# Kernel tuning notes

Hardware: AMD Instinct MI355X
Metric: run time of the kernel (lower is better)

## Reference

```python
import jax, jax.numpy as jnp
import numpy as np
import math

MODEL_DIM = 1024
HEAD_DIM = 64
NUM_HEADS = 16
FF_MULT = 4
FF_DIM = FF_MULT * MODEL_DIM
ATTN_DIM = NUM_HEADS * HEAD_DIM
FUSED_DIMS = (ATTN_DIM, ATTN_DIM, ATTN_DIM, FF_DIM, FF_DIM)


def setup_inputs() -> dict:
    key = jax.random.key(0)
    k_x, k_in, k_attn, k_ff = jax.random.split(key, 4)
    B, S = 2, 2048
    inputs = jax.random.normal(k_x, (B, S, MODEL_DIM), dtype=jnp.float32)
    # LayerNorm affine params (torch defaults: weight=1, bias=0)
    ln_w = jnp.ones((MODEL_DIM,), dtype=jnp.float32)
    ln_b = jnp.zeros((MODEL_DIM,), dtype=jnp.float32)
    # Linear weights stored as [in, out] (equivalent to torch W.T)
    s_in = 1.0 / math.sqrt(MODEL_DIM)
    w_in = jax.random.uniform(k_in, (MODEL_DIM, sum(FUSED_DIMS)), jnp.float32, -s_in, s_in)
    s_a = 1.0 / math.sqrt(ATTN_DIM)
    w_attn = jax.random.uniform(k_attn, (ATTN_DIM, MODEL_DIM), jnp.float32, -s_a, s_a)
    s_f = 1.0 / math.sqrt(FF_DIM)
    w_ff = jax.random.uniform(k_ff, (FF_DIM, MODEL_DIM), jnp.float32, -s_f, s_f)
    return {"inputs": inputs, "ln_w": ln_w, "ln_b": ln_b,
            "w_in": w_in, "w_attn": w_attn, "w_ff": w_ff}


def _layer_norm(x, w, b, eps=1e-5):
    mu = jnp.mean(x, axis=-1, keepdims=True)
    var = jnp.var(x, axis=-1, keepdims=True)
    return (x - mu) * jax.lax.rsqrt(var + eps) * w + b


def reference(inputs, ln_w, ln_b, w_in, w_attn, w_ff):
    B, S, D = inputs.shape
    units = _layer_norm(inputs, ln_w, ln_b)
    proj = units @ w_in                                   # [B,S,3*A+2*F]
    splits = np.cumsum(FUSED_DIMS)[:-1]
    q, k, v, ff, ff_gate = jnp.split(proj, splits, axis=-1)
    # split heads: [B,S,H*d] -> [B,H,S,d]
    def heads(t):
        return t.reshape(B, S, NUM_HEADS, HEAD_DIM).transpose(0, 2, 1, 3)
    q, k, v = heads(q), heads(k), heads(v)
    scale = 1.0 / math.sqrt(HEAD_DIM)
    score = jnp.einsum('bhsd,bhTd->bhsT', q, k) * scale   # [B,H,S,S]
    weight = jax.nn.softmax(score, axis=-1)
    attn = jnp.einsum('bhsT,bhTd->bhsd', weight, v)       # [B,H,S,d]
    concat = attn.transpose(0, 2, 1, 3).reshape(B, S, ATTN_DIM)
    attn_out = concat @ w_attn                            # [B,S,D]
    ff_out = (ff * jax.nn.gelu(ff_gate, approximate=True)) @ w_ff
    return inputs + attn_out + ff_out
```

## Files before the change

kernel.cpp:

```cpp
#include <hip/hip_runtime.h>
#include <hip/hip_bf16.h>
#include <cstdint>
#include <cstddef>

typedef __bf16 bf16;
typedef __bf16 bf16x8 __attribute__((ext_vector_type(8)));
typedef float f32x4 __attribute__((ext_vector_type(4)));

#define MFMA16(a, b, c) __builtin_amdgcn_mfma_f32_16x16x32_bf16(a, b, c, 0, 0, 0)

#define GLOBAL_LOAD_LDS16(gptr, lptr)                                          \
  __builtin_amdgcn_global_load_lds(                                            \
      (const __attribute__((address_space(1))) void*)(gptr),                   \
      (__attribute__((address_space(3))) void*)(lptr), 16, 0, 0)

__global__ void transpose_all(const float* __restrict__ w_in,
                              const float* __restrict__ w_attn,
                              const float* __restrict__ w_ff,
                              bf16* __restrict__ wt_in,
                              bf16* __restrict__ wtcat) {
  __shared__ float t[32][33];
  int id = blockIdx.x;
  const float* src; bf16* dst;
  int srcN, srccol0, LDO, mode, obase, goff, kcol0, ntn;
  if (id < 3072) {
    src = w_in; dst = wt_in; srcN = 11264; srccol0 = 0; LDO = 1024;
    mode = 0; obase = 0; goff = 0; kcol0 = 0; ntn = 96;
  } else if (id < 7168) {
    id -= 3072; src = w_in; dst = wt_in; srcN = 11264; srccol0 = 3072;
    LDO = 1024; mode = 1; obase = 3072; goff = 0; kcol0 = 0; ntn = 128;
  } else if (id < 11264) {
    id -= 7168; src = w_in; dst = wt_in; srcN = 11264; srccol0 = 7168;
    LDO = 1024; mode = 1; obase = 3072; goff = 64; kcol0 = 0; ntn = 128;
  } else if (id < 12288) {
    id -= 11264; src = w_attn; dst = wtcat; srcN = 1024; srccol0 = 0;
    LDO = 5120; mode = 0; obase = 0; goff = 0; kcol0 = 0; ntn = 32;
  } else {
    id -= 12288; src = w_ff; dst = wtcat; srcN = 1024; srccol0 = 0;
    LDO = 5120; mode = 0; obase = 0; goff = 0; kcol0 = 1024; ntn = 32;
  }
  const int n0 = (id % ntn) * 32, k0 = (id / ntn) * 32;
  const int tx = threadIdx.x, ty = threadIdx.y;
  for (int i = ty; i < 32; i += 8)
    t[i][tx] = src[(size_t)(k0 + i) * srcN + srccol0 + n0 + tx];
  __syncthreads();
  for (int i = ty; i < 32; i += 8) {
    int n = n0 + i;
    int orow = mode ? (obase + ((n >> 6) << 7) + goff + (n & 63)) : (obase + n);
    dst[(size_t)orow * LDO + kcol0 + k0 + tx] = (bf16)t[tx][i];
  }
}

__global__ __launch_bounds__(256) void lnorm(const float* __restrict__ x,
                                             const float* __restrict__ w,
                                             const float* __restrict__ b,
                                             bf16* __restrict__ y) {
  const int row = blockIdx.x;
  const int tid = threadIdx.x;
  const float* xr = x + (size_t)row * 1024;
  float4 v = *(const float4*)&xr[tid * 4];
  float s = v.x + v.y + v.z + v.w;
  float ss = v.x * v.x + v.y * v.y + v.z * v.z + v.w * v.w;
  __shared__ float rs[256], rss[256];
  rs[tid] = s; rss[tid] = ss;
  __syncthreads();
  for (int off = 128; off > 0; off >>= 1) {
    if (tid < off) { rs[tid] += rs[tid + off]; rss[tid] += rss[tid + off]; }
    __syncthreads();
  }
  const float mean = rs[0] * (1.f / 1024.f);
  const float var = rss[0] * (1.f / 1024.f) - mean * mean;
  const float rstd = rsqrtf(var + 1e-5f);
  const float* vp = (const float*)&v;
  for (int i = 0; i < 4; i++) {
    int c = tid * 4 + i;
    y[(size_t)row * 1024 + c] = (bf16)((vp[i] - mean) * rstd * w[c] + b[c]);
  }
}

__global__ __launch_bounds__(256) void vtrans(const bf16* __restrict__ proj,
                                              bf16* __restrict__ vt) {
  __shared__ bf16 t[64][80];
  const int tid = threadIdx.x;
  const int s0 = blockIdx.x * 64;
  const int h = blockIdx.y, b = blockIdx.z;
  constexpr size_t LDP = 3072;
  const bf16* src = proj + (size_t)b * 2048 * LDP + 2048 + h * 64;
  {
    int s = tid >> 2, d0 = (tid & 3) * 16;
    *(bf16x8*)&t[s][d0]     = *(const bf16x8*)&src[(size_t)(s0 + s) * LDP + d0];
    *(bf16x8*)&t[s][d0 + 8] = *(const bf16x8*)&src[(size_t)(s0 + s) * LDP + d0 + 8];
  }
  __syncthreads();
  {
    int d = tid >> 2, sb = (tid & 3) * 16;
    bf16* dst = vt + ((size_t)(b * 16 + h) * 64 + d) * 2048 + s0 + sb;
    bf16x8 o0, o1;
    for (int i = 0; i < 8; i++) { o0[i] = t[sb + i][d]; o1[i] = t[sb + 8 + i][d]; }
    *(bf16x8*)&dst[0] = o0;
    *(bf16x8*)&dst[8] = o1;
  }
}

__global__ __launch_bounds__(256) void flash_attn(const bf16* __restrict__ proj,
                                                  const bf16* __restrict__ vt,
                                                  bf16* __restrict__ hcat) {
  __shared__ __align__(16) char smem[50176];
  bf16* Ks = (bf16*)smem;
  bf16* Vs = (bf16*)(smem + 16384);
  bf16* Ps = (bf16*)(smem + 32768);
  const int tid = threadIdx.x;
  const int wave = tid >> 6, lane = tid & 63;
  const int quad = lane >> 4, l16 = lane & 15;
  const int q0 = blockIdx.x * 64;
  const int h = blockIdx.y, b = blockIdx.z;
  constexpr size_t LDP = 3072;
  const bf16* Qb = proj + (size_t)b * 2048 * LDP + h * 64;
  const bf16* Kb = proj + (size_t)b * 2048 * LDP + 1024 + h * 64;
  const bf16* Vt = vt + (size_t)(b * 16 + h) * 64 * 2048;

  const int qrow = q0 + wave * 16 + l16;
  bf16x8 aq0r = *(const bf16x8*)&Qb[(size_t)qrow * LDP + quad * 8];
  bf16x8 aq1r = *(const bf16x8*)&Qb[(size_t)qrow * LDP + 32 + quad * 8];
  bf16x8 aq0, aq1;
#pragma unroll
  for (int i = 0; i < 8; i++) {
    aq0[i] = (bf16)((float)aq0r[i] * 0.125f);
    aq1[i] = (bf16)((float)aq1r[i] * 0.125f);
  }

  f32x4 O[4] = {};
  float lrow[4] = {0.f, 0.f, 0.f, 0.f};

  const int krow = wave * 8 + (lane >> 3);
  const int kq   = ((lane & 7) ^ ((lane >> 3) & 7)) * 8;
  const int kslot = (lane & 7) * 8;
  const int vrow = wave * 4 + (lane >> 4);
  const int vq   = ((lane & 15) ^ ((wave * 4 + (lane >> 4)) & 7)) * 8;
  const int vslot = (lane & 15) * 8;
  const int ks0 = (quad ^ (l16 & 7)) * 8;
  const int ks1 = ((quad + 4) ^ (l16 & 7)) * 8;

  for (int j0 = 0; j0 < 2048; j0 += 128) {
#pragma unroll
    for (int p = 0; p < 4; p++) {
      int kr = p * 32 + krow;
      GLOBAL_LOAD_LDS16(&Kb[(size_t)(j0 + kr) * LDP + kq], &Ks[kr * 64 + kslot]);
      int vr = p * 16 + vrow;
      GLOBAL_LOAD_LDS16(&Vt[(size_t)vr * 2048 + j0 + vq], &Vs[vr * 128 + vslot]);
    }
    __syncthreads();

    f32x4 sa[8];
#pragma unroll
    for (int nt = 0; nt < 8; nt++) {
      bf16x8 bk0 = *(const bf16x8*)&Ks[(nt * 16 + l16) * 64 + ks0];
      bf16x8 bk1 = *(const bf16x8*)&Ks[(nt * 16 + l16) * 64 + ks1];
      f32x4 t = {};
      t = MFMA16(aq0, bk0, t);
      sa[nt] = MFMA16(aq1, bk1, t);
    }

    bf16* Pw = Ps + wave * (16 * 136);
#pragma unroll
    for (int r = 0; r < 4; r++) {
      bf16* pr = &Pw[(quad * 4 + r) * 136];
      float ts = 0.f;
#pragma unroll
      for (int nt = 0; nt < 8; nt++) {
        float p = __expf(sa[nt][r]);
        pr[nt * 16 + l16] = (bf16)p;
        ts += p;
      }
#pragma unroll
      for (int d = 1; d < 16; d <<= 1) ts += __shfl_xor(ts, d, 64);
      lrow[r] += ts;
    }

#pragma unroll
    for (int kg = 0; kg < 4; kg++) {
      bf16x8 aP = *(const bf16x8*)&Pw[l16 * 136 + kg * 32 + quad * 8];
#pragma unroll
      for (int nb = 0; nb < 4; nb++) {
        int vrr = nb * 16 + l16;
        int vsl = (((kg * 4 + quad) ^ (l16 & 7))) * 8;
        bf16x8 bv = *(const bf16x8*)&Vs[vrr * 128 + vsl];
        O[nb] = MFMA16(aP, bv, O[nb]);
      }
    }
    __syncthreads();
  }

#pragma unroll
  for (int r = 0; r < 4; r++) {
    float inv = 1.f / lrow[r];
    size_t row = (size_t)b * 2048 + q0 + wave * 16 + quad * 4 + r;
#pragma unroll
    for (int nb = 0; nb < 4; nb++)
      hcat[row * 5120 + h * 64 + nb * 16 + l16] = (bf16)(O[nb][r] * inv);
  }
}

__global__ __launch_bounds__(256) void gemm_proj(const bf16* __restrict__ A,
                                                 const bf16* __restrict__ Bt,
                                                 bf16* __restrict__ proj,
                                                 bf16* __restrict__ hcat) {
  constexpr int K = 1024, LDC = 136;
  __shared__ __align__(16) char smem[17408];
  bf16* As = (bf16*)smem;
  bf16* Bs = As + 128 * 32;
  bf16* Cs = (bf16*)smem;
  const int tid = threadIdx.x;
  const int wave = tid >> 6, lane = tid & 63;
  const int quad = lane >> 4, l16 = lane & 15;
  constexpr int NM = 4, NN = 4;
  const int wm0 = (wave >> 1) * 64, wn0 = (wave & 1) * 64;
  const size_t rowA0 = (size_t)blockIdx.y * 128;
  const size_t rowB0 = (size_t)blockIdx.x * 128;

  const int srow = wave * 16 + (lane >> 2);
  const int sq = ((lane & 3) ^ ((lane >> 3) & 3)) * 8;
  const int sslot = (lane & 3) * 8;
  const int rslot = (quad ^ ((l16 >> 1) & 3)) * 8;

  f32x4 acc[NM][NN] = {};

  for (int k0 = 0; k0 < K; k0 += 32) {
#pragma unroll
    for (int p = 0; p < 2; p++) {
      int r = p * 64 + srow;
      GLOBAL_LOAD_LDS16(&A[(rowA0 + r) * K + k0 + sq], &As[r * 32 + sslot]);
      GLOBAL_LOAD_LDS16(&Bt[(rowB0 + r) * K + k0 + sq], &Bs[r * 32 + sslot]);
    }
    __syncthreads();
    bf16x8 af[NM], bfr[NN];
#pragma unroll
    for (int i = 0; i < NM; i++)
      af[i] = *(const bf16x8*)&As[(wm0 + i * 16 + l16) * 32 + rslot];
#pragma unroll
    for (int j = 0; j < NN; j++)
      bfr[j] = *(const bf16x8*)&Bs[(wn0 + j * 16 + l16) * 32 + rslot];
#pragma unroll
    for (int i = 0; i < NM; i++)
#pragma unroll
      for (int j = 0; j < NN; j++)
        acc[i][j] = MFMA16(af[i], bfr[j], acc[i][j]);
    __syncthreads();
  }

#pragma unroll
  for (int half = 0; half < 2; half++) {
    if ((wave >> 1) == half) {
#pragma unroll
      for (int i = 0; i < NM; i++)
#pragma unroll
        for (int j = 0; j < NN; j++)
#pragma unroll
          for (int r = 0; r < 4; r++)
            Cs[(i * 16 + quad * 4 + r) * LDC + wn0 + j * 16 + l16] =
                (bf16)acc[i][j][r];
    }
    __syncthreads();
    if (blockIdx.x < 24) {
      const int c0 = (tid & 15) * 8;
#pragma unroll
      for (int it = 0; it < 4; it++) {
        int row = (tid >> 4) + it * 16;
        *(bf16x8*)&proj[(rowA0 + half * 64 + row) * 3072 + rowB0 + c0] =
            *(const bf16x8*)&Cs[row * LDC + c0];
      }
    } else {
      const int T = blockIdx.x - 24;
      const int c0 = (tid & 7) * 8;
#pragma unroll
      for (int p = 0; p < 2; p++) {
        int row = (tid >> 3) + p * 32;
        bf16x8 f = *(const bf16x8*)&Cs[row * LDC + c0];
        bf16x8 g = *(const bf16x8*)&Cs[row * LDC + 64 + c0];
        bf16x8 o;
#pragma unroll
        for (int i = 0; i < 8; i++) {
          float xg = (float)g[i];
          float u = 0.7978845608f * (xg + 0.044715f * xg * xg * xg);
          float gl = xg / (1.f + __expf(-2.f * u));
          o[i] = (bf16)((float)f[i] * gl);
        }
        *(bf16x8*)&hcat[(rowA0 + half * 64 + row) * 5120 + 1024 + T * 64 + c0] = o;
      }
    }
    __syncthreads();
  }
}

__global__ __launch_bounds__(256) void gemm_out(const bf16* __restrict__ A,
                                                const bf16* __restrict__ Bt,
                                                bf16* __restrict__ part) {
  constexpr int LDAB = 5120, LDC = 136;
  __shared__ __align__(16) char smem[17408];
  bf16* As = (bf16*)smem;
  bf16* Bs = As + 128 * 32;
  bf16* Cs = (bf16*)smem;
  const int tid = threadIdx.x;
  const int wave = tid >> 6, lane = tid & 63;
  const int quad = lane >> 4, l16 = lane & 15;
  constexpr int NM = 4, NN = 4;
  const int wm0 = (wave >> 1) * 64, wn0 = (wave & 1) * 64;
  const size_t rowA0 = (size_t)blockIdx.y * 128;
  const size_t rowB0 = (size_t)blockIdx.x * 128;
  const int kbeg = blockIdx.z * 1280, kend = kbeg + 1280;

  const int srow = wave * 16 + (lane >> 2);
  const int sq = ((lane & 3) ^ ((lane >> 3) & 3)) * 8;
  const int sslot = (lane & 3) * 8;
  const int rslot = (quad ^ ((l16 >> 1) & 3)) * 8;

  f32x4 acc[NM][NN] = {};

  for (int k0 = kbeg; k0 < kend; k0 += 32) {
#pragma unroll
    for (int p = 0; p < 2; p++) {
      int r = p * 64 + srow;
      GLOBAL_LOAD_LDS16(&A[(rowA0 + r) * LDAB + k0 + sq], &As[r * 32 + sslot]);
      GLOBAL_LOAD_LDS16(&Bt[(rowB0 + r) * LDAB + k0 + sq], &Bs[r * 32 + sslot]);
    }
    __syncthreads();
    bf16x8 af[NM], bfr[NN];
#pragma unroll
    for (int i = 0; i < NM; i++)
      af[i] = *(const bf16x8*)&As[(wm0 + i * 16 + l16) * 32 + rslot];
#pragma unroll
    for (int j = 0; j < NN; j++)
      bfr[j] = *(const bf16x8*)&Bs[(wn0 + j * 16 + l16) * 32 + rslot];
#pragma unroll
    for (int i = 0; i < NM; i++)
#pragma unroll
      for (int j = 0; j < NN; j++)
        acc[i][j] = MFMA16(af[i], bfr[j], acc[i][j]);
    __syncthreads();
  }

  bf16* dst = part + (size_t)blockIdx.z * (4096 * 1024);
#pragma unroll
  for (int half = 0; half < 2; half++) {
    if ((wave >> 1) == half) {
#pragma unroll
      for (int i = 0; i < NM; i++)
#pragma unroll
        for (int j = 0; j < NN; j++)
#pragma unroll
          for (int r = 0; r < 4; r++)
            Cs[(i * 16 + quad * 4 + r) * LDC + wn0 + j * 16 + l16] =
                (bf16)acc[i][j][r];
    }
    __syncthreads();
    const int c0 = (tid & 15) * 8;
#pragma unroll
    for (int it = 0; it < 4; it++) {
      int row = (tid >> 4) + it * 16;
      *(bf16x8*)&dst[(rowA0 + half * 64 + row) * 1024 + rowB0 + c0] =
          *(const bf16x8*)&Cs[row * LDC + c0];
    }
    __syncthreads();
  }
}

__global__ __launch_bounds__(256) void reduce_out(const float* __restrict__ x,
                                                  const bf16* __restrict__ part,
                                                  float* __restrict__ out) {
  const size_t i = ((size_t)blockIdx.x * 256 + threadIdx.x) * 8;
  constexpr size_t SL = 4096 * 1024;
  float r[8];
  float4 x0 = *(const float4*)&x[i];
  float4 x1 = *(const float4*)&x[i + 4];
  r[0] = x0.x; r[1] = x0.y; r[2] = x0.z; r[3] = x0.w;
  r[4] = x1.x; r[5] = x1.y; r[6] = x1.z; r[7] = x1.w;
#pragma unroll
  for (int z = 0; z < 4; z++) {
    bf16x8 p = *(const bf16x8*)&part[z * SL + i];
#pragma unroll
    for (int k = 0; k < 8; k++) r[k] += (float)p[k];
  }
  float4 o0 = {r[0], r[1], r[2], r[3]};
  float4 o1 = {r[4], r[5], r[6], r[7]};
  *(float4*)&out[i] = o0;
  *(float4*)&out[i + 4] = o1;
}

extern "C" void kernel_launch(void* const* d_in, const int* in_sizes, int n_in,
                              void* d_out, int out_size, void* d_ws, size_t ws_size,
                              hipStream_t stream) {
  const float* x      = (const float*)d_in[0];
  const float* ln_w   = (const float*)d_in[1];
  const float* ln_b   = (const float*)d_in[2];
  const float* w_in   = (const float*)d_in[3];
  const float* w_attn = (const float*)d_in[4];
  const float* w_ff   = (const float*)d_in[5];
  float* out = (float*)d_out;
  char* ws = (char*)d_ws;

  bf16* wt_in = (bf16*)(ws);
  bf16* wtcat = (bf16*)(ws + 23068672);
  bf16* xn    = (bf16*)(ws + 33554432);
  bf16* proj  = (bf16*)(ws + 41943040);
  bf16* part  = (bf16*)(ws + 67108864);
  bf16* vt    = (bf16*)(ws + 100663296);
  bf16* hcat  = (bf16*)(ws + 134217728);

  transpose_all<<<16384, dim3(32, 8), 0, stream>>>(w_in, w_attn, w_ff, wt_in, wtcat);
  lnorm<<<4096, 256, 0, stream>>>(x, ln_w, ln_b, xn);
  gemm_proj<<<dim3(88, 32), 256, 0, stream>>>(xn, wt_in, proj, hcat);
  vtrans<<<dim3(32, 16, 2), 256, 0, stream>>>(proj, vt);
  flash_attn<<<dim3(32, 16, 2), 256, 0, stream>>>(proj, vt, hcat);
  gemm_out<<<dim3(8, 32, 4), 256, 0, stream>>>(hcat, wtcat, part);
  reduce_out<<<2048, 256, 0, stream>>>(x, part, out);
}
```

Baseline: 432.8 us.

## Fuse V transpose into projection epilogue and use 32x32 MFMA attention

The projection GEMM epilogue now writes V directly in transposed layout, which removes the separate vtrans kernel and its round trip through global memory. Q/K stay in a narrower proj buffer. The flash attention kernel is rewritten to use 32x32x16 MFMA tiles with 128 query rows per block and 32 per wave, swizzled LDS layouts, and a row-sum reduction deferred to the end. The risks are fewer blocks (512) and higher register and LDS use per block. The transposed epilogue also does strided column reads from LDS.

Result: slower. 459.7 us (+6.2%).

```diff
diff --git a/kernel.cpp b/kernel.cpp
--- a/kernel.cpp
+++ b/kernel.cpp
@@ -6,8 +6,10 @@
 typedef __bf16 bf16;
 typedef __bf16 bf16x8 __attribute__((ext_vector_type(8)));
 typedef float f32x4 __attribute__((ext_vector_type(4)));
+typedef float f32x16 __attribute__((ext_vector_type(16)));
 
 #define MFMA16(a, b, c) __builtin_amdgcn_mfma_f32_16x16x32_bf16(a, b, c, 0, 0, 0)
+#define MFMA32(a, b, c) __builtin_amdgcn_mfma_f32_32x32x16_bf16(a, b, c, 0, 0, 0)
 
 #define GLOBAL_LOAD_LDS16(gptr, lptr)                                          \
   __builtin_amdgcn_global_load_lds(                                            \
@@ -78,132 +80,116 @@
   }
 }
 
-__global__ __launch_bounds__(256) void vtrans(const bf16* __restrict__ proj,
-                                              bf16* __restrict__ vt) {
-  __shared__ bf16 t[64][80];
-  const int tid = threadIdx.x;
-  const int s0 = blockIdx.x * 64;
-  const int h = blockIdx.y, b = blockIdx.z;
-  constexpr size_t LDP = 3072;
-  const bf16* src = proj + (size_t)b * 2048 * LDP + 2048 + h * 64;
-  {
-    int s = tid >> 2, d0 = (tid & 3) * 16;
-    *(bf16x8*)&t[s][d0]     = *(const bf16x8*)&src[(size_t)(s0 + s) * LDP + d0];
-    *(bf16x8*)&t[s][d0 + 8] = *(const bf16x8*)&src[(size_t)(s0 + s) * LDP + d0 + 8];
-  }
-  __syncthreads();
-  {
-    int d = tid >> 2, sb = (tid & 3) * 16;
-    bf16* dst = vt + ((size_t)(b * 16 + h) * 64 + d) * 2048 + s0 + sb;
-    bf16x8 o0, o1;
-    for (int i = 0; i < 8; i++) { o0[i] = t[sb + i][d]; o1[i] = t[sb + 8 + i][d]; }
-    *(bf16x8*)&dst[0] = o0;
-    *(bf16x8*)&dst[8] = o1;
-  }
-}
-
 __global__ __launch_bounds__(256) void flash_attn(const bf16* __restrict__ proj,
                                                   const bf16* __restrict__ vt,
                                                   bf16* __restrict__ hcat) {
-  __shared__ __align__(16) char smem[50176];
+  __shared__ __align__(16) char smem[65536];
   bf16* Ks = (bf16*)smem;
   bf16* Vs = (bf16*)(smem + 16384);
   bf16* Ps = (bf16*)(smem + 32768);
   const int tid = threadIdx.x;
   const int wave = tid >> 6, lane = tid & 63;
-  const int quad = lane >> 4, l16 = lane & 15;
-  const int q0 = blockIdx.x * 64;
+  const int l32 = lane & 31, half = lane >> 5;
+  const int q0 = blockIdx.x * 128;
   const int h = blockIdx.y, b = blockIdx.z;
-  constexpr size_t LDP = 3072;
+  constexpr size_t LDP = 2048;
   const bf16* Qb = proj + (size_t)b * 2048 * LDP + h * 64;
   const bf16* Kb = proj + (size_t)b * 2048 * LDP + 1024 + h * 64;
   const bf16* Vt = vt + (size_t)(b * 16 + h) * 64 * 2048;
 
-  const int qrow = q0 + wave * 16 + l16;
-  bf16x8 aq0r = *(const bf16x8*)&Qb[(size_t)qrow * LDP + quad * 8];
-  bf16x8 aq1r = *(const bf16x8*)&Qb[(size_t)qrow * LDP + 32 + quad * 8];
-  bf16x8 aq0, aq1;
-#pragma unroll
-  for (int i = 0; i < 8; i++) {
-    aq0[i] = (bf16)((float)aq0r[i] * 0.125f);
-    aq1[i] = (bf16)((float)aq1r[i] * 0.125f);
-  }
-
-  f32x4 O[4] = {};
-  float lrow[4] = {0.f, 0.f, 0.f, 0.f};
-
-  const int krow = wave * 8 + (lane >> 3);
-  const int kq   = ((lane & 7) ^ ((lane >> 3) & 7)) * 8;
-  const int kslot = (lane & 7) * 8;
-  const int vrow = wave * 4 + (lane >> 4);
-  const int vq   = ((lane & 15) ^ ((wave * 4 + (lane >> 4)) & 7)) * 8;
-  const int vslot = (lane & 15) * 8;
-  const int ks0 = (quad ^ (l16 & 7)) * 8;
-  const int ks1 = ((quad + 4) ^ (l16 & 7)) * 8;
+  const int qrow = q0 + wave * 32 + l32;
+  bf16x8 aq[4];
+#pragma unroll
+  for (int c = 0; c < 4; c++) {
+    bf16x8 r = *(const bf16x8*)&Qb[(size_t)qrow * LDP + c * 16 + half * 8];
+#pragma unroll
+    for (int i = 0; i < 8; i++) aq[c][i] = (bf16)((float)r[i] * 0.125f);
+  }
+
+  f32x16 O0 = {}, O1 = {};
+  float psum[16];
+#pragma unroll
+  for (int i = 0; i < 16; i++) psum[i] = 0.f;
+
+  const int krow_ = wave * 8 + (lane >> 3);
+  const int kq_ = ((lane & 7) ^ (krow_ & 7)) * 8;
+  const int vrow_ = wave * 4 + (lane >> 4);
+  const int vq_ = ((lane & 15) ^ (vrow_ & 15)) * 8;
+  bf16* Pw = Ps + wave * (32 * 128);
 
   for (int j0 = 0; j0 < 2048; j0 += 128) {
 #pragma unroll
     for (int p = 0; p < 4; p++) {
-      int kr = p * 32 + krow;
-      GLOBAL_LOAD_LDS16(&Kb[(size_t)(j0 + kr) * LDP + kq], &Ks[kr * 64 + kslot]);
-      int vr = p * 16 + vrow;
-      GLOBAL_LOAD_LDS16(&Vt[(size_t)vr * 2048 + j0 + vq], &Vs[vr * 128 + vslot]);
-    }
-    __syncthreads();
-
-    f32x4 sa[8];
-#pragma unroll
-    for (int nt = 0; nt < 8; nt++) {
-      bf16x8 bk0 = *(const bf16x8*)&Ks[(nt * 16 + l16) * 64 + ks0];
-      bf16x8 bk1 = *(const bf16x8*)&Ks[(nt * 16 + l16) * 64 + ks1];
-      f32x4 t = {};
-      t = MFMA16(aq0, bk0, t);
-      sa[nt] = MFMA16(aq1, bk1, t);
-    }
-
-    bf16* Pw = Ps + wave * (16 * 136);
-#pragma unroll
-    for (int r = 0; r < 4; r++) {
-      bf16* pr = &Pw[(quad * 4 + r) * 136];
-      float ts = 0.f;
-#pragma unroll
-      for (int nt = 0; nt < 8; nt++) {
-        float p = __expf(sa[nt][r]);
-        pr[nt * 16 + l16] = (bf16)p;
-        ts += p;
-      }
-#pragma unroll
-      for (int d = 1; d < 16; d <<= 1) ts += __shfl_xor(ts, d, 64);
-      lrow[r] += ts;
-    }
-
-#pragma unroll
-    for (int kg = 0; kg < 4; kg++) {
-      bf16x8 aP = *(const bf16x8*)&Pw[l16 * 136 + kg * 32 + quad * 8];
-#pragma unroll
-      for (int nb = 0; nb < 4; nb++) {
-        int vrr = nb * 16 + l16;
-        int vsl = (((kg * 4 + quad) ^ (l16 & 7))) * 8;
-        bf16x8 bv = *(const bf16x8*)&Vs[vrr * 128 + vsl];
-        O[nb] = MFMA16(aP, bv, O[nb]);
-      }
-    }
-    __syncthreads();
-  }
-
-#pragma unroll
-  for (int r = 0; r < 4; r++) {
-    float inv = 1.f / lrow[r];
-    size_t row = (size_t)b * 2048 + q0 + wave * 16 + quad * 4 + r;
-#pragma unroll
-    for (int nb = 0; nb < 4; nb++)
-      hcat[row * 5120 + h * 64 + nb * 16 + l16] = (bf16)(O[nb][r] * inv);
+      int kr = p * 32 + krow_;
+      GLOBAL_LOAD_LDS16(&Kb[(size_t)(j0 + kr) * LDP + kq_],
+                        &Ks[kr * 64 + (lane & 7) * 8]);
+      int vr = p * 16 + vrow_;
+      GLOBAL_LOAD_LDS16(&Vt[(size_t)vr * 2048 + j0 + vq_],
+                        &Vs[vr * 128 + (lane & 15) * 8]);
+    }
+    __syncthreads();
+
+    f32x16 sacc[4];
+#pragma unroll
+    for (int g = 0; g < 4; g++) {
+      f32x16 t = {};
+      int r = g * 32 + l32;
+#pragma unroll
+      for (int c = 0; c < 4; c++) {
+        int sl = (c * 2 + half) ^ (r & 7);
+        bf16x8 bk = *(const bf16x8*)&Ks[r * 64 + sl * 8];
+        t = MFMA32(aq[c], bk, t);
+      }
+      sacc[g] = t;
+    }
+
+#pragma unroll
+    for (int g = 0; g < 4; g++) {
+#pragma unroll
+      for (int reg = 0; reg < 16; reg++) {
+        float p = __expf(sacc[g][reg]);
+        psum[reg] += p;
+        int pr = (reg & 3) + 8 * (reg >> 2) + 4 * half;
+        int pc = g * 32 + l32;
+        Pw[pr * 128 + ((pc >> 3) ^ (pr & 15)) * 8 + (pc & 7)] = (bf16)p;
+      }
+    }
+
+#pragma unroll
+    for (int c = 0; c < 8; c++) {
+      int sl = (c * 2 + half) ^ (l32 & 15);
+      bf16x8 aP = *(const bf16x8*)&Pw[l32 * 128 + sl * 8];
+      {
+        bf16x8 bv = *(const bf16x8*)&Vs[l32 * 128 + sl * 8 + 0];
+        O0 = MFMA32(aP, bv, O0);
+      }
+      {
+        int vr = 32 + l32;
+        int vsl = (c * 2 + half) ^ (vr & 15);
+        bf16x8 bv = *(const bf16x8*)&Vs[vr * 128 + vsl * 8];
+        O1 = MFMA32(aP, bv, O1);
+      }
+    }
+    __syncthreads();
+  }
+
+#pragma unroll
+  for (int reg = 0; reg < 16; reg++) {
+    float ts = psum[reg];
+#pragma unroll
+    for (int d = 1; d < 32; d <<= 1) ts += __shfl_xor(ts, d, 64);
+    float inv = 1.f / ts;
+    int qr = (reg & 3) + 8 * (reg >> 2) + 4 * half;
+    size_t row = (size_t)b * 2048 + q0 + wave * 32 + qr;
+    hcat[row * 5120 + h * 64 + l32] = (bf16)(O0[reg] * inv);
+    hcat[row * 5120 + h * 64 + 32 + l32] = (bf16)(O1[reg] * inv);
   }
 }
 
 __global__ __launch_bounds__(256) void gemm_proj(const bf16* __restrict__ A,
                                                  const bf16* __restrict__ Bt,
                                                  bf16* __restrict__ proj,
+                                                 bf16* __restrict__ vt,
                                                  bf16* __restrict__ hcat) {
   constexpr int K = 1024, LDC = 136;
   __shared__ __align__(16) char smem[17408];
@@ -261,14 +247,25 @@
                 (bf16)acc[i][j][r];
     }
     __syncthreads();
-    if (blockIdx.x < 24) {
+    if (blockIdx.x < 16) {
       const int c0 = (tid & 15) * 8;
 #pragma unroll
       for (int it = 0; it < 4; it++) {
         int row = (tid >> 4) + it * 16;
-        *(bf16x8*)&proj[(rowA0 + half * 64 + row) * 3072 + rowB0 + c0] =
+        *(bf16x8*)&proj[(rowA0 + half * 64 + row) * 2048 + rowB0 + c0] =
             *(const bf16x8*)&Cs[row * LDC + c0];
       }
+    } else if (blockIdx.x < 24) {
+      const int cl = tid >> 1;
+      const int so = (tid & 1) * 32;
+      const size_t vtrow = (rowA0 >> 11) * 1024 + rowB0 - 2048 + cl;
+      const int sbase = (int)(rowA0 & 2047) + half * 64 + so;
+      bf16 v[32];
+#pragma unroll
+      for (int i = 0; i < 32; i++) v[i] = Cs[(so + i) * LDC + cl];
+      bf16* dst = vt + vtrow * 2048 + sbase;
+#pragma unroll
+      for (int k = 0; k < 4; k++) *(bf16x8*)&dst[k * 8] = *(bf16x8*)&v[k * 8];
     } else {
       const int T = blockIdx.x - 24;
       const int c0 = (tid & 7) * 8;
@@ -408,9 +405,8 @@
 
   transpose_all<<<16384, dim3(32, 8), 0, stream>>>(w_in, w_attn, w_ff, wt_in, wtcat);
   lnorm<<<4096, 256, 0, stream>>>(x, ln_w, ln_b, xn);
-  gemm_proj<<<dim3(88, 32), 256, 0, stream>>>(xn, wt_in, proj, hcat);
-  vtrans<<<dim3(32, 16, 2), 256, 0, stream>>>(proj, vt);
-  flash_attn<<<dim3(32, 16, 2), 256, 0, stream>>>(proj, vt, hcat);
+  gemm_proj<<<dim3(88, 32), 256, 0, stream>>>(xn, wt_in, proj, vt, hcat);
+  flash_attn<<<dim3(16, 16, 2), 256, 0, stream>>>(proj, vt, hcat);
   gemm_out<<<dim3(8, 32, 4), 256, 0, stream>>>(hcat, wtcat, part);
   reduce_out<<<2048, 256, 0, stream>>>(x, part, out);
 }
```
